# Performance work log

Hardware: AMD Instinct MI355X
Metric: run time of the kernel (lower is better)

Reference implementation:

```python
import jax, jax.numpy as jnp
import numpy as np

B = 32768
STEPS = 20
WIDTH = 48
RADIUS = 0.1
LR = 0.1          # inner Adam lr
B1, B2, ADAM_EPS = 0.9, 0.999, 1e-8
Y_MEAN = 0.0


def _uniform(key, shape, lim):
    return jax.random.uniform(key, shape, minval=-lim, maxval=lim, dtype=jnp.float32)


def setup_inputs() -> dict:
    key = jax.random.key(0)
    ks = jax.random.split(key, 10)
    # x in the data range [-1.5, 1.5]
    x = jax.random.uniform(ks[0], (B, 1), minval=-1.5, maxval=1.5, dtype=jnp.float32)
    # per-step, per-sample epsilon ~ U(-radius, radius)
    eps = jax.random.uniform(ks[1], (STEPS, B, 1), minval=-RADIUS, maxval=RADIUS, dtype=jnp.float32)
    # equinox MLP init: U(-1/sqrt(in), 1/sqrt(in)) for weights and biases
    l1 = 1.0 / np.sqrt(2.0)
    lw = 1.0 / np.sqrt(WIDTH)
    W1 = _uniform(ks[2], (WIDTH, 2), l1); b1 = _uniform(ks[3], (WIDTH,), l1)
    W2 = _uniform(ks[4], (WIDTH, WIDTH), lw); b2 = _uniform(ks[5], (WIDTH,), lw)
    W3 = _uniform(ks[6], (WIDTH, WIDTH), lw); b3 = _uniform(ks[7], (WIDTH,), lw)
    W4 = _uniform(ks[8], (1, WIDTH), lw); b4 = _uniform(ks[9], (1,), lw)
    return {"x": x, "eps": eps, "W1": W1, "b1": b1, "W2": W2, "b2": b2,
            "W3": W3, "b3": b3, "W4": W4, "b4": b4}


def reference(x, eps, W1, b1, W2, b2, W3, b3, W4, b4):
    # sum over batch of energies; per-sample grads decouple since samples are independent
    def energy_sum(y):  # y: [B,1]
        inp = jnp.concatenate([x, y], axis=-1)              # [B,2]
        h = jax.nn.swish(inp @ W1.T + b1)                   # [B,48]
        h = jax.nn.swish(h @ W2.T + b2)
        h = jax.nn.swish(h @ W3.T + b3)
        return (h @ W4.T + b4).sum()

    grad_fn = jax.grad(energy_sum)  # [B,1] -> [B,1]

    def step(carry, inp):
        y, m, v = carry
        t, eps_i = inp
        y0 = y + eps_i                                      # perturbed Taylor anchor
        # grad of 2nd-order Taylor expansion of E around y0, evaluated at y:
        #   E'(y0) + E''(y0) * (y - y0)
        g1 = grad_fn(y0)
        _, hvp = jax.jvp(grad_fn, (y0,), (y - y0,))
        g = g1 + hvp
        # optax.adam(0.1) update
        m = B1 * m + (1.0 - B1) * g
        v = B2 * v + (1.0 - B2) * (g * g)
        mhat = m / (1.0 - jnp.power(B1, t))
        vhat = v / (1.0 - jnp.power(B2, t))
        y = y - LR * mhat / (jnp.sqrt(vhat) + ADAM_EPS)
        return (y, m, v), None

    y_init = jnp.full((B, 1), Y_MEAN, dtype=x.dtype)
    m0 = jnp.zeros_like(y_init)
    v0 = jnp.zeros_like(y_init)
    ts = jnp.arange(1, STEPS + 1, dtype=x.dtype)            # Adam step counts
    (y_final, _, _), _ = jax.lax.scan(step, (y_init, m0, v0), (ts, eps))
    return y_final  # [B,1]
```

## Files before the change

kernel.cpp:

```cpp
#include <hip/hip_runtime.h>

namespace {

typedef _Float16 half8 __attribute__((ext_vector_type(8)));
typedef float    f32x4 __attribute__((ext_vector_type(4)));

constexpr int BATCH = 32768;
constexpr int STEPS = 20;
constexpr int WD    = 48;
constexpr int SPW   = 16;
constexpr int AKW   = 72;
constexpr float LR   = 0.1f;
constexpr float B1C  = 0.9f;
constexpr float B2C  = 0.999f;
constexpr float AEPS = 1e-8f;

__device__ __forceinline__ void swish3(float z, float& a, float& d1, float& d2) {
    const float sg = 1.f / (1.f + __expf(-z));
    const float sp = sg * (1.f - sg);
    d1 = fmaf(z, sp, sg);
    d2 = sp * fmaf(z, 1.f - 2.f * sg, 2.f);
    a  = z * sg;
}

__global__ __launch_bounds__(64, 2) void ebm_kernel(
    const float* __restrict__ x_in,  const float* __restrict__ eps_in,
    const float* __restrict__ W1,    const float* __restrict__ b1,
    const float* __restrict__ W2,    const float* __restrict__ b2,
    const float* __restrict__ W3,    const float* __restrict__ b3,
    const float* __restrict__ W4,
    float* __restrict__ out)
{
    const int lane = threadIdx.x & 63;
    const int c    = lane & 15;
    const int g    = lane >> 4;
    const int s0   = blockIdx.x * SPW;
    const int sc   = s0 + c;
    const bool hiv = (g < 2);

    __shared__ __attribute__((aligned(16))) _Float16 Ah[3][SPW][AKW];
    __shared__ float2 pdS[SPW];

    float w1x[16], w1y[16], b1r[16];
#pragma unroll
    for (int j = 0; j < 8; ++j) {
        const int u = 8 * g + j;
        w1x[j] = W1[2 * u]; w1y[j] = W1[2 * u + 1]; b1r[j] = b1[u];
    }
#pragma unroll
    for (int j = 0; j < 8; ++j) {
        const int u = 32 + 8 * g + j;
        w1x[8 + j] = hiv ? W1[2 * u]     : 0.f;
        w1y[8 + j] = hiv ? W1[2 * u + 1] : 0.f;
        b1r[8 + j] = hiv ? b1[u]         : 0.f;
    }

    half8 bfr[2][3][2];
#pragma unroll
    for (int lay = 0; lay < 2; ++lay) {
        const float* __restrict__ Wsrc = lay ? W3 : W2;
#pragma unroll
        for (int tn = 0; tn < 3; ++tn) {
#pragma unroll
            for (int kc = 0; kc < 2; ++kc) {
                const int i  = tn * 16 + c;
                const int k0 = kc * 32 + g * 8;
                half8 h;
#pragma unroll
                for (int j = 0; j < 8; ++j) h[j] = (_Float16)0.f;
                if (k0 < WD) {
                    const float* src = Wsrc + i * WD + k0;
#pragma unroll
                    for (int j = 0; j < 8; ++j) h[j] = (_Float16)src[j];
                }
                bfr[lay][tn][kc] = h;
            }
        }
    }

    float w4r[3], b2r[3], b3r[3];
#pragma unroll
    for (int tn = 0; tn < 3; ++tn) {
        const int i = tn * 16 + c;
        w4r[tn] = W4[i]; b2r[tn] = b2[i]; b3r[tn] = b3[i];
    }

    const float xv = x_in[sc];
    float y = 0.f, m = 0.f, v = 0.f;
    float pb1 = 1.f, pb2 = 1.f;

#pragma unroll 1
    for (int t = 0; t < STEPS; ++t) {
        const float e  = eps_in[t * BATCH + sc];
        const float y0 = y + e;
        pb1 *= B1C; pb2 *= B2C;

        half8 af[3][2];
#pragma unroll
        for (int kc = 0; kc < 2; ++kc) {
#pragma unroll
            for (int j = 0; j < 8; ++j) {
                const int sl = kc * 8 + j;
                const float z1 = fmaf(w1y[sl], y0, fmaf(w1x[sl], xv, b1r[sl]));
                float a, d1, d2; swish3(z1, a, d1, d2);
                af[0][kc][j] = (_Float16)a;
                af[1][kc][j] = (_Float16)(d1 * w1y[sl]);
                af[2][kc][j] = (_Float16)(d2 * w1y[sl] * w1y[sl]);
            }
        }

        f32x4 acc[3][3];
#pragma unroll
        for (int ch = 0; ch < 3; ++ch)
#pragma unroll
            for (int tn = 0; tn < 3; ++tn) {
                acc[ch][tn] = f32x4{0.f, 0.f, 0.f, 0.f};
#pragma unroll
                for (int kc = 0; kc < 2; ++kc)
                    acc[ch][tn] = __builtin_amdgcn_mfma_f32_16x16x32_f16(
                        af[ch][kc], bfr[0][tn][kc], acc[ch][tn], 0, 0, 0);
            }

        asm volatile("" ::: "memory");
#pragma unroll
        for (int tn = 0; tn < 3; ++tn) {
#pragma unroll
            for (int r = 0; r < 4; ++r) {
                const float z  = acc[0][tn][r] + b2r[tn];
                const float zp = acc[1][tn][r];
                const float zq = acc[2][tn][r];
                float a, d1, d2; swish3(z, a, d1, d2);
                const int row = 4 * g + r;
                const int col = 16 * tn + c;
                Ah[0][row][col] = (_Float16)a;
                Ah[1][row][col] = (_Float16)(d1 * zp);
                Ah[2][row][col] = (_Float16)fmaf(d2 * zp, zp, d1 * zq);
            }
        }
        asm volatile("s_waitcnt lgkmcnt(0)" ::: "memory");
        __builtin_amdgcn_sched_barrier(0);

#pragma unroll
        for (int ch = 0; ch < 3; ++ch) {
            af[ch][0] = *reinterpret_cast<const half8*>(&Ah[ch][c][8 * g]);
            half8 z8;
#pragma unroll
            for (int j = 0; j < 8; ++j) z8[j] = (_Float16)0.f;
            if (hiv) z8 = *reinterpret_cast<const half8*>(&Ah[ch][c][32 + 8 * g]);
            af[ch][1] = z8;
        }

#pragma unroll
        for (int ch = 0; ch < 3; ++ch)
#pragma unroll
            for (int tn = 0; tn < 3; ++tn) {
                acc[ch][tn] = f32x4{0.f, 0.f, 0.f, 0.f};
#pragma unroll
                for (int kc = 0; kc < 2; ++kc)
                    acc[ch][tn] = __builtin_amdgcn_mfma_f32_16x16x32_f16(
                        af[ch][kc], bfr[1][tn][kc], acc[ch][tn], 0, 0, 0);
            }

        float pd1[4] = {0.f, 0.f, 0.f, 0.f};
        float pd2[4] = {0.f, 0.f, 0.f, 0.f};
#pragma unroll
        for (int tn = 0; tn < 3; ++tn) {
#pragma unroll
            for (int r = 0; r < 4; ++r) {
                const float z  = acc[0][tn][r] + b3r[tn];
                const float zp = acc[1][tn][r];
                const float zq = acc[2][tn][r];
                float a, d1, d2; swish3(z, a, d1, d2);
                pd1[r] = fmaf(w4r[tn], d1 * zp, pd1[r]);
                pd2[r] = fmaf(w4r[tn], fmaf(d2 * zp, zp, d1 * zq), pd2[r]);
            }
        }
#pragma unroll
        for (int off = 1; off < 16; off <<= 1) {
#pragma unroll
            for (int r = 0; r < 4; ++r) {
                pd1[r] += __shfl_xor(pd1[r], off);
                pd2[r] += __shfl_xor(pd2[r], off);
            }
        }
        asm volatile("" ::: "memory");
        if (c < 4) {
            const float a1 = (c == 0) ? pd1[0] : (c == 1) ? pd1[1] : (c == 2) ? pd1[2] : pd1[3];
            const float a2 = (c == 0) ? pd2[0] : (c == 1) ? pd2[1] : (c == 2) ? pd2[2] : pd2[3];
            pdS[4 * g + c] = make_float2(a1, a2);
        }
        asm volatile("s_waitcnt lgkmcnt(0)" ::: "memory");
        __builtin_amdgcn_sched_barrier(0);
        const float2 pd = pdS[c];

        const float gg = fmaf(pd.y, -e, pd.x);
        m = fmaf(B1C, m, (1.f - B1C) * gg);
        v = fmaf(B2C, v, (1.f - B2C) * gg * gg);
        const float mh = m / (1.f - pb1);
        const float vh = v / (1.f - pb2);
        y -= LR * mh / (sqrtf(vh) + AEPS);
    }

    if (g == 0) out[sc] = y;
}

}

extern "C" void kernel_launch(void* const* d_in, const int* in_sizes, int n_in,
                              void* d_out, int out_size, void* d_ws, size_t ws_size,
                              hipStream_t stream) {
    const float* x   = (const float*)d_in[0];
    const float* eps = (const float*)d_in[1];
    const float* W1  = (const float*)d_in[2];
    const float* b1  = (const float*)d_in[3];
    const float* W2  = (const float*)d_in[4];
    const float* b2  = (const float*)d_in[5];
    const float* W3  = (const float*)d_in[6];
    const float* b3  = (const float*)d_in[7];
    const float* W4  = (const float*)d_in[8];
    float* out = (float*)d_out;

    ebm_kernel<<<BATCH / SPW, 64, 0, stream>>>(x, eps, W1, b1, W2, b2, W3, b3, W4, out);
}
```

Baseline: 179.1 us.

## Rebalance layer-1 hidden units across lane groups and trim per-step overheads

Spreads the 48 first-layer hidden units evenly as 12 per lane group instead of 16/16/8/8, and permutes the LDS column layout to match so no lane computes padded zero units. Packs fp16 conversions with cvt_pkrtz, replaces divisions with hardware reciprocal and sqrt intrinsics, prefetches the next step's eps, and swaps the LDS round-trip for the per-sample gradient with a cross-lane shuffle. The cost is reduced precision from approximate reciprocal and round-toward-zero packing, plus a more intricate column mapping that must stay consistent with the zero-padded weight fragments.

```diff
diff --git a/kernel.cpp b/kernel.cpp
--- a/kernel.cpp
+++ b/kernel.cpp
@@ -2,8 +2,10 @@
 
 namespace {
 
-typedef _Float16 half8 __attribute__((ext_vector_type(8)));
-typedef float    f32x4 __attribute__((ext_vector_type(4)));
+typedef _Float16 half8  __attribute__((ext_vector_type(8)));
+typedef _Float16 half2v __attribute__((ext_vector_type(2)));
+typedef float    f32x4  __attribute__((ext_vector_type(4)));
+typedef unsigned int uint4v __attribute__((ext_vector_type(4)));
 
 constexpr int BATCH = 32768;
 constexpr int STEPS = 20;
@@ -16,7 +18,7 @@
 constexpr float AEPS = 1e-8f;
 
 __device__ __forceinline__ void swish3(float z, float& a, float& d1, float& d2) {
-    const float sg = 1.f / (1.f + __expf(-z));
+    const float sg = __builtin_amdgcn_rcpf(1.f + __expf(-z));
     const float sp = sg * (1.f - sg);
     d1 = fmaf(z, sp, sg);
     d2 = sp * fmaf(z, 1.f - 2.f * sg, 2.f);
@@ -34,25 +36,20 @@
     const int lane = threadIdx.x & 63;
     const int c    = lane & 15;
     const int g    = lane >> 4;
-    const int s0   = blockIdx.x * SPW;
-    const int sc   = s0 + c;
-    const bool hiv = (g < 2);
+    const int sc   = blockIdx.x * SPW + c;
 
     __shared__ __attribute__((aligned(16))) _Float16 Ah[3][SPW][AKW];
-    __shared__ float2 pdS[SPW];
-
-    float w1x[16], w1y[16], b1r[16];
-#pragma unroll
-    for (int j = 0; j < 8; ++j) {
-        const int u = 8 * g + j;
+
+    {
+        unsigned int* p = reinterpret_cast<unsigned int*>(&Ah[0][0][0]);
+        for (int i = lane; i < 3 * SPW * AKW / 2; i += 64) p[i] = 0u;
+    }
+
+    float w1x[12], w1y[12], b1r[12];
+#pragma unroll
+    for (int j = 0; j < 12; ++j) {
+        const int u = 12 * g + j;
         w1x[j] = W1[2 * u]; w1y[j] = W1[2 * u + 1]; b1r[j] = b1[u];
-    }
-#pragma unroll
-    for (int j = 0; j < 8; ++j) {
-        const int u = 32 + 8 * g + j;
-        w1x[8 + j] = hiv ? W1[2 * u]     : 0.f;
-        w1y[8 + j] = hiv ? W1[2 * u + 1] : 0.f;
-        b1r[8 + j] = hiv ? b1[u]         : 0.f;
     }
 
     half8 bfr[2][3][2];
@@ -61,53 +58,84 @@
         const float* __restrict__ Wsrc = lay ? W3 : W2;
 #pragma unroll
         for (int tn = 0; tn < 3; ++tn) {
-#pragma unroll
-            for (int kc = 0; kc < 2; ++kc) {
-                const int i  = tn * 16 + c;
-                const int k0 = kc * 32 + g * 8;
-                half8 h;
-#pragma unroll
-                for (int j = 0; j < 8; ++j) h[j] = (_Float16)0.f;
-                if (k0 < WD) {
-                    const float* src = Wsrc + i * WD + k0;
-#pragma unroll
-                    for (int j = 0; j < 8; ++j) h[j] = (_Float16)src[j];
-                }
-                bfr[lay][tn][kc] = h;
-            }
+            const int col = 16 * tn + c;
+#pragma unroll
+            for (int j = 0; j < 8; ++j)
+                bfr[lay][tn][0][j] = (_Float16)Wsrc[col * WD + 12 * g + j];
+#pragma unroll
+            for (int j = 0; j < 4; ++j)
+                bfr[lay][tn][1][j] = (_Float16)Wsrc[col * WD + 12 * g + 8 + j];
+#pragma unroll
+            for (int j = 4; j < 8; ++j)
+                bfr[lay][tn][1][j] = (_Float16)0.f;
         }
     }
 
     float w4r[3], b2r[3], b3r[3];
+    int colw[3];
 #pragma unroll
     for (int tn = 0; tn < 3; ++tn) {
-        const int i = tn * 16 + c;
-        w4r[tn] = W4[i]; b2r[tn] = b2[i]; b3r[tn] = b3[i];
-    }
+        const int u = 16 * tn + c;
+        w4r[tn] = W4[u]; b2r[tn] = b2[u]; b3r[tn] = b3[u];
+        const int gu  = u / 12;
+        const int rem = u - 12 * gu;
+        const int kcu = rem >> 3;
+        colw[tn] = 32 * kcu + 8 * gu + (rem - 8 * kcu);
+    }
+
+#pragma unroll
+    for (int l = 0; l < 2; ++l)
+#pragma unroll
+        for (int tn = 0; tn < 3; ++tn)
+#pragma unroll
+            for (int kc = 0; kc < 2; ++kc)
+                asm volatile("" : "+v"(bfr[l][tn][kc]));
+#pragma unroll
+    for (int j = 0; j < 12; ++j)
+        asm volatile("" : "+v"(w1x[j]), "+v"(w1y[j]), "+v"(b1r[j]));
+#pragma unroll
+    for (int tn = 0; tn < 3; ++tn)
+        asm volatile("" : "+v"(w4r[tn]), "+v"(b2r[tn]), "+v"(b3r[tn]));
 
     const float xv = x_in[sc];
     float y = 0.f, m = 0.f, v = 0.f;
     float pb1 = 1.f, pb2 = 1.f;
+    float e = eps_in[sc];
 
 #pragma unroll 1
     for (int t = 0; t < STEPS; ++t) {
-        const float e  = eps_in[t * BATCH + sc];
+        const int tn1 = (t + 1 < STEPS) ? t + 1 : STEPS - 1;
+        const float e_nxt = eps_in[tn1 * BATCH + sc];
         const float y0 = y + e;
         pb1 *= B1C; pb2 *= B2C;
 
+        uint4v afu[3][2];
+#pragma unroll
+        for (int jp = 0; jp < 6; ++jp) {
+            const int s0 = 2 * jp, s1 = 2 * jp + 1;
+            float a0, d10, d20, a1, d11, d21;
+            const float z0 = fmaf(w1y[s0], y0, fmaf(w1x[s0], xv, b1r[s0]));
+            const float z1 = fmaf(w1y[s1], y0, fmaf(w1x[s1], xv, b1r[s1]));
+            swish3(z0, a0, d10, d20);
+            swish3(z1, a1, d11, d21);
+            const int kc = jp >> 2, wrd = jp & 3;
+            afu[0][kc][wrd] = __builtin_bit_cast(unsigned int,
+                __builtin_amdgcn_cvt_pkrtz(a0, a1));
+            afu[1][kc][wrd] = __builtin_bit_cast(unsigned int,
+                __builtin_amdgcn_cvt_pkrtz(d10 * w1y[s0], d11 * w1y[s1]));
+            afu[2][kc][wrd] = __builtin_bit_cast(unsigned int,
+                __builtin_amdgcn_cvt_pkrtz(d20 * w1y[s0] * w1y[s0],
+                                           d21 * w1y[s1] * w1y[s1]));
+        }
+#pragma unroll
+        for (int ch = 0; ch < 3; ++ch) { afu[ch][1][2] = 0u; afu[ch][1][3] = 0u; }
+
         half8 af[3][2];
 #pragma unroll
-        for (int kc = 0; kc < 2; ++kc) {
-#pragma unroll
-            for (int j = 0; j < 8; ++j) {
-                const int sl = kc * 8 + j;
-                const float z1 = fmaf(w1y[sl], y0, fmaf(w1x[sl], xv, b1r[sl]));
-                float a, d1, d2; swish3(z1, a, d1, d2);
-                af[0][kc][j] = (_Float16)a;
-                af[1][kc][j] = (_Float16)(d1 * w1y[sl]);
-                af[2][kc][j] = (_Float16)(d2 * w1y[sl] * w1y[sl]);
-            }
-        }
+        for (int ch = 0; ch < 3; ++ch)
+#pragma unroll
+            for (int kc = 0; kc < 2; ++kc)
+                af[ch][kc] = __builtin_bit_cast(half8, afu[ch][kc]);
 
         f32x4 acc[3][3];
 #pragma unroll
@@ -131,10 +159,9 @@
                 const float zq = acc[2][tn][r];
                 float a, d1, d2; swish3(z, a, d1, d2);
                 const int row = 4 * g + r;
-                const int col = 16 * tn + c;
-                Ah[0][row][col] = (_Float16)a;
-                Ah[1][row][col] = (_Float16)(d1 * zp);
-                Ah[2][row][col] = (_Float16)fmaf(d2 * zp, zp, d1 * zq);
+                Ah[0][row][colw[tn]] = (_Float16)a;
+                Ah[1][row][colw[tn]] = (_Float16)(d1 * zp);
+                Ah[2][row][colw[tn]] = (_Float16)fmaf(d2 * zp, zp, d1 * zq);
             }
         }
         asm volatile("s_waitcnt lgkmcnt(0)" ::: "memory");
@@ -143,11 +170,7 @@
 #pragma unroll
         for (int ch = 0; ch < 3; ++ch) {
             af[ch][0] = *reinterpret_cast<const half8*>(&Ah[ch][c][8 * g]);
-            half8 z8;
-#pragma unroll
-            for (int j = 0; j < 8; ++j) z8[j] = (_Float16)0.f;
-            if (hiv) z8 = *reinterpret_cast<const half8*>(&Ah[ch][c][32 + 8 * g]);
-            af[ch][1] = z8;
+            af[ch][1] = *reinterpret_cast<const half8*>(&Ah[ch][c][32 + 8 * g]);
         }
 
 #pragma unroll
@@ -183,22 +206,20 @@
                 pd2[r] += __shfl_xor(pd2[r], off);
             }
         }
-        asm volatile("" ::: "memory");
-        if (c < 4) {
-            const float a1 = (c == 0) ? pd1[0] : (c == 1) ? pd1[1] : (c == 2) ? pd1[2] : pd1[3];
-            const float a2 = (c == 0) ? pd2[0] : (c == 1) ? pd2[1] : (c == 2) ? pd2[2] : pd2[3];
-            pdS[4 * g + c] = make_float2(a1, a2);
-        }
-        asm volatile("s_waitcnt lgkmcnt(0)" ::: "memory");
-        __builtin_amdgcn_sched_barrier(0);
-        const float2 pd = pdS[c];
-
-        const float gg = fmaf(pd.y, -e, pd.x);
+        const int c3 = c & 3;
+        const float s1 = (c3 == 0) ? pd1[0] : (c3 == 1) ? pd1[1] : (c3 == 2) ? pd1[2] : pd1[3];
+        const float s2 = (c3 == 0) ? pd2[0] : (c3 == 1) ? pd2[1] : (c3 == 2) ? pd2[2] : pd2[3];
+        const int src = ((c >> 2) << 4) | c;
+        const float gd1 = __shfl(s1, src, 64);
+        const float gd2 = __shfl(s2, src, 64);
+
+        const float gg = fmaf(gd2, -e, gd1);
         m = fmaf(B1C, m, (1.f - B1C) * gg);
         v = fmaf(B2C, v, (1.f - B2C) * gg * gg);
-        const float mh = m / (1.f - pb1);
-        const float vh = v / (1.f - pb2);
-        y -= LR * mh / (sqrtf(vh) + AEPS);
+        const float mh = m * __builtin_amdgcn_rcpf(1.f - pb1);
+        const float vh = v * __builtin_amdgcn_rcpf(1.f - pb2);
+        y -= LR * mh * __builtin_amdgcn_rcpf(__builtin_amdgcn_sqrtf(vh) + AEPS);
+        e = e_nxt;
     }
 
     if (g == 0) out[sc] = y;
```

Result: faster. 148.8 us (-16.9%).
